# Kernel tuning notes

Hardware: AMD Instinct MI355X
Metric: run time of the kernel (lower is better)

## Reference

```python
import jax, jax.numpy as jnp
import numpy as np

B, F, C = 16384, 256, 256


def setup_inputs() -> dict:
    key = jax.random.key(0)
    ks = jax.random.split(key, 10)
    return {
        "x_t": jax.random.normal(ks[0], (B, F), dtype=jnp.float32),
        "n_t": jax.random.normal(ks[1], (B, C), dtype=jnp.float32),
        "d_t": jax.random.uniform(ks[2], (B, C), dtype=jnp.float32),
        "h_t": jax.random.normal(ks[3], (B, C), dtype=jnp.float32),
        "a_max_t": jax.random.normal(ks[4], (B, C), dtype=jnp.float32),
        "Wu": jax.random.normal(ks[5], (C, F), dtype=jnp.float32) * 0.06,
        "bu": jnp.zeros((C,), dtype=jnp.float32),
        "Wg": jax.random.normal(ks[6], (C, F + C), dtype=jnp.float32) * 0.05,
        "bg": jnp.zeros((C,), dtype=jnp.float32),
        "Wa": jax.random.normal(ks[7], (C, F + C), dtype=jnp.float32) * 0.05,
        "Wd": jax.random.normal(ks[8], (C, F + C), dtype=jnp.float32) * 0.05,
    }


def reference(x_t, n_t, d_t, h_t, a_max_t, Wu, bu, Wg, bg, Wa, Wd):
    # xh_join = cat([x_t, h_t], dim=1) -> [B, F+C]
    xh = jnp.concatenate([x_t, h_t], axis=1)
    u_t = x_t @ Wu.T + bu                      # [B, C]
    g_t = xh @ Wg.T + bg                       # [B, C]
    a_t = xh @ Wa.T                            # [B, C] (no bias)
    z_t = u_t * jnp.tanh(g_t)
    # decay branch (self.decay is an nn.Linear -> always truthy in original)
    decay = jax.nn.sigmoid(xh @ Wd.T)
    e_neg = jnp.exp(-decay)
    a_decay = a_max_t * e_neg
    a_newmax = jnp.maximum(a_decay, a_t)
    exp_diff = jnp.exp(a_max_t - a_newmax)
    exp_scaled = jnp.exp(a_t - a_newmax)
    n_new = n_t * e_neg * exp_diff + z_t * exp_scaled
    d_new = d_t * e_neg * exp_diff + exp_scaled
    h_new = jnp.tanh(n_new / d_new)
    return (n_new, d_new, h_new, a_newmax)
```

## Files before the change

### kernel.cpp

```cpp
#include <hip/hip_runtime.h>
#include <stdint.h>

typedef _Float16 f16x8 __attribute__((ext_vector_type(8)));
typedef __fp16 fp16x2 __attribute__((ext_vector_type(2)));
typedef float f32x4 __attribute__((ext_vector_type(4)));

#define BC (16384 * 256)

__device__ __forceinline__ f16x8 cvt8(f32x4 a, f32x4 b) {
  fp16x2 p0 = __builtin_amdgcn_cvt_pkrtz(a[0], a[1]);
  fp16x2 p1 = __builtin_amdgcn_cvt_pkrtz(a[2], a[3]);
  fp16x2 p2 = __builtin_amdgcn_cvt_pkrtz(b[0], b[1]);
  fp16x2 p3 = __builtin_amdgcn_cvt_pkrtz(b[2], b[3]);
  f16x8 o;
  o[0] = (_Float16)p0[0]; o[1] = (_Float16)p0[1];
  o[2] = (_Float16)p1[0]; o[3] = (_Float16)p1[1];
  o[4] = (_Float16)p2[0]; o[5] = (_Float16)p2[1];
  o[6] = (_Float16)p3[0]; o[7] = (_Float16)p3[1];
  return o;
}

__device__ __forceinline__ float tanh_fast(float v) {
  float a = fminf(fabsf(v), 18.f);
  float t = __expf(2.f * a);
  float r = (t - 1.f) * __builtin_amdgcn_rcpf(t + 1.f);
  return copysignf(r, v);
}

__global__ __launch_bounds__(256) void pack_w(const float* __restrict__ Wu,
                                              const float* __restrict__ Wg,
                                              const float* __restrict__ Wa,
                                              const float* __restrict__ Wd,
                                              _Float16* __restrict__ wsB) {
  int t = blockIdx.x * 256 + threadIdx.x;
  int slot = t & 7;
  int kt = (t >> 3) & 7;
  int row = (t >> 6) & 127;
  int cb = t >> 13;
  int strip = (row >> 4) & 3;
  int wn = row >> 6;
  int t16 = row & 15;
  int c = cb * 32 + wn * 16 + t16;
  int k0 = kt * 64 + (slot ^ (row & 7)) * 8;
  float v[8];
  if (strip == 0) {
    if (k0 < 256) {
      const float* p = Wu + (size_t)c * 256 + k0;
#pragma unroll
      for (int i = 0; i < 8; ++i) v[i] = p[i];
    } else {
#pragma unroll
      for (int i = 0; i < 8; ++i) v[i] = 0.f;
    }
  } else {
    const float* p = (strip == 1 ? Wg : (strip == 2 ? Wa : Wd)) + (size_t)c * 512 + k0;
#pragma unroll
    for (int i = 0; i < 8; ++i) v[i] = p[i];
  }
  f32x4 a = {v[0], v[1], v[2], v[3]};
  f32x4 b = {v[4], v[5], v[6], v[7]};
  *reinterpret_cast<f16x8*>(wsB + (size_t)cb * 65536 + row * 512 + kt * 64 + slot * 8) =
      cvt8(a, b);
}

__global__ __launch_bounds__(256, 3) void rwa_main(
    const float* __restrict__ x, const float* __restrict__ nt_,
    const float* __restrict__ dt_, const float* __restrict__ h,
    const float* __restrict__ amax_, const float* __restrict__ bu,
    const float* __restrict__ bg, const _Float16* __restrict__ wsB,
    float* __restrict__ out) {
  __shared__ __align__(16) _Float16 ldsA[2][64 * 64];
  __shared__ __align__(16) _Float16 ldsB[2][128 * 64];

  const int tid = threadIdx.x;
  const int lane = tid & 63;
  const int l15 = lane & 15;
  const int lg = lane >> 4;
  const int wv = tid >> 6;
  const int wm = wv & 1;
  const int wn = wv >> 1;

  const int bid = blockIdx.x;
  const int xcd = bid & 7;
  const int q = bid >> 3;
  const int cb = q & 7;
  const int rowblk = xcd * 32 + (q >> 3);
  const int row0 = rowblk * 64;

  const int ar = tid >> 2;
  const int aq = tid & 3;

  const _Float16* bsrc0 = wsB + (size_t)cb * 65536 + (tid >> 3) * 512 + (tid & 7) * 8;

  f32x4 acc[2][4] = {};
  f32x4 av[4];

  auto issueA = [&](int kt) {
    const float* sp = (kt < 4 ? x : h) + (size_t)(row0 + ar) * 256 + (kt & 3) * 64 + aq * 16;
#pragma unroll
    for (int i = 0; i < 4; ++i) av[i] = *reinterpret_cast<const f32x4*>(sp + i * 4);
  };
  auto issueB = [&](int buf, int kt) {
#pragma unroll
    for (int i = 0; i < 4; ++i) {
      __builtin_amdgcn_global_load_lds(
          (const __attribute__((address_space(1))) uint32_t*)(bsrc0 + (size_t)kt * 64 + i * 16384),
          (__attribute__((address_space(3))) uint32_t*)(&ldsB[buf][0] + wv * 512 + i * 2048),
          16, 0, 0);
    }
  };
  auto writeA = [&](int buf) {
#pragma unroll
    for (int j = 0; j < 2; ++j) {
      f16x8 o = cvt8(av[2 * j], av[2 * j + 1]);
      const int slot = (aq * 2 + j) ^ (ar & 7);
      *reinterpret_cast<f16x8*>(reinterpret_cast<char*>(&ldsA[buf][0]) + ar * 128 + slot * 16) = o;
    }
  };

  issueA(0);
  issueB(0, 0);
  writeA(0);
  __syncthreads();

#pragma unroll
  for (int kt = 0; kt < 8; ++kt) {
    const int buf = kt & 1;
    if (kt < 7) {
      issueA(kt + 1);
      issueB(buf ^ 1, kt + 1);
    }

    const bool doU = (kt < 4);
    const char* pA = reinterpret_cast<const char*>(&ldsA[buf][0]);
    const char* pB = reinterpret_cast<const char*>(&ldsB[buf][0]);
    const int rswz = (l15 & 7) << 4;
#pragma unroll
    for (int ks = 0; ks < 2; ++ks) {
      f16x8 af[2], bf[4];
#pragma unroll
      for (int mi = 0; mi < 2; ++mi) {
        const int row = wm * 32 + mi * 16 + l15;
        af[mi] = *reinterpret_cast<const f16x8*>(pA + row * 128 + ((ks * 64 + lg * 16) ^ rswz));
      }
#pragma unroll
      for (int s = 0; s < 4; ++s) {
        if (s == 0 && !doU) continue;
        const int pc = wn * 64 + s * 16 + l15;
        bf[s] = *reinterpret_cast<const f16x8*>(pB + pc * 128 + ((ks * 64 + lg * 16) ^ rswz));
      }
#pragma unroll
      for (int s = 0; s < 4; ++s) {
        if (s == 0 && !doU) continue;
#pragma unroll
        for (int mi = 0; mi < 2; ++mi)
          acc[mi][s] = __builtin_amdgcn_mfma_f32_16x16x32_f16(af[mi], bf[s], acc[mi][s], 0, 0, 0);
      }
    }

    if (kt < 7) {
      writeA(buf ^ 1);
      __syncthreads();
    }
  }

  const int c = cb * 32 + wn * 16 + l15;
  const float buv = bu[c];
  const float bgv = bg[c];
#pragma unroll
  for (int mi = 0; mi < 2; ++mi) {
#pragma unroll
    for (int rg = 0; rg < 4; ++rg) {
      const int r = row0 + wm * 32 + mi * 16 + lg * 4 + rg;
      const int idx = r * 256 + c;
      const float u = acc[mi][0][rg] + buv;
      const float gt = acc[mi][1][rg] + bgv;
      const float a = acc[mi][2][rg];
      const float dr = acc[mi][3][rg];
      const float sig = __builtin_amdgcn_rcpf(1.f + __expf(-dr));
      const float z = u * tanh_fast(gt);
      const float am = amax_[idx];
      const float n_old = nt_[idx];
      const float d_old = dt_[idx];
      const float e_neg = __expf(-sig);
      const float a_new = fmaxf(am * e_neg, a);
      const float comm = __expf(am - a_new - sig);
      const float escal = __expf(a - a_new);
      const float n_new = n_old * comm + z * escal;
      const float d_new = d_old * comm + escal;
      const float h_new = tanh_fast(n_new * __builtin_amdgcn_rcpf(d_new));
      out[idx] = n_new;
      out[BC + idx] = d_new;
      out[2 * BC + idx] = h_new;
      out[3 * BC + idx] = a_new;
    }
  }
}

extern "C" void kernel_launch(void* const* d_in, const int* in_sizes, int n_in,
                              void* d_out, int out_size, void* d_ws, size_t ws_size,
                              hipStream_t stream) {
  const float* x_t    = (const float*)d_in[0];
  const float* n_t    = (const float*)d_in[1];
  const float* d_t    = (const float*)d_in[2];
  const float* h_t    = (const float*)d_in[3];
  const float* amax_t = (const float*)d_in[4];
  const float* Wu     = (const float*)d_in[5];
  const float* bu     = (const float*)d_in[6];
  const float* Wg     = (const float*)d_in[7];
  const float* bg     = (const float*)d_in[8];
  const float* Wa     = (const float*)d_in[9];
  const float* Wd     = (const float*)d_in[10];
  float* out = (float*)d_out;

  _Float16* wsB = (_Float16*)d_ws;

  pack_w<<<256, 256, 0, stream>>>(Wu, Wg, Wa, Wd, wsB);
  rwa_main<<<2048, 256, 0, stream>>>(x_t, n_t, d_t, h_t, amax_t, bu, bg, wsB, out);
}
```

Before: 52.88 us.

## Pre-pack activations to swizzled fp16 and stream A tiles via direct-to-LDS loads

Adds a pack_a kernel that converts x and h to fp16 in the swizzled tile layout the GEMM expects, stored in workspace. The main kernel then loads A tiles with global_load_lds like B, replacing the register load, convert and LDS write path. Explicit vmcnt waits and raw barriers replace __syncthreads to overlap the next tile's loads with compute. This costs an extra kernel launch and a full read and write pass over the activations. Each A tile is now read by 8 column-block workgroups in half-size fp16 rather than fp32.

Measured after the change: 51.95 us. No clear change (-1.8%).

```diff
diff --git a/kernel.cpp b/kernel.cpp
--- a/kernel.cpp
+++ b/kernel.cpp
@@ -63,12 +63,27 @@
       cvt8(a, b);
 }
 
+__global__ __launch_bounds__(256) void pack_a(const float* __restrict__ x,
+                                              const float* __restrict__ h,
+                                              _Float16* __restrict__ wsA) {
+  int tid = blockIdx.x * 256 + threadIdx.x;
+  int slot = tid & 7;
+  int row6 = (tid >> 3) & 63;
+  int kt = (tid >> 9) & 7;
+  int rb = tid >> 12;
+  int rowg = rb * 64 + row6;
+  int kin = (kt & 3) * 64 + (slot ^ (row6 & 7)) * 8;
+  const float* src = (kt < 4 ? x : h) + (size_t)rowg * 256 + kin;
+  f32x4 a = *reinterpret_cast<const f32x4*>(src);
+  f32x4 b = *reinterpret_cast<const f32x4*>(src + 4);
+  *reinterpret_cast<f16x8*>(wsA + (size_t)tid * 8) = cvt8(a, b);
+}
+
 __global__ __launch_bounds__(256, 3) void rwa_main(
-    const float* __restrict__ x, const float* __restrict__ nt_,
-    const float* __restrict__ dt_, const float* __restrict__ h,
+    const float* __restrict__ nt_, const float* __restrict__ dt_,
     const float* __restrict__ amax_, const float* __restrict__ bu,
-    const float* __restrict__ bg, const _Float16* __restrict__ wsB,
-    float* __restrict__ out) {
+    const float* __restrict__ bg, const _Float16* __restrict__ wsA,
+    const _Float16* __restrict__ wsB, float* __restrict__ out) {
   __shared__ __align__(16) _Float16 ldsA[2][64 * 64];
   __shared__ __align__(16) _Float16 ldsB[2][128 * 64];
 
@@ -87,20 +102,19 @@
   const int rowblk = xcd * 32 + (q >> 3);
   const int row0 = rowblk * 64;
 
-  const int ar = tid >> 2;
-  const int aq = tid & 3;
-
+  const _Float16* asrc0 = wsA + (size_t)rowblk * 32768 + (size_t)tid * 8;
   const _Float16* bsrc0 = wsB + (size_t)cb * 65536 + (tid >> 3) * 512 + (tid & 7) * 8;
 
   f32x4 acc[2][4] = {};
-  f32x4 av[4];
-
-  auto issueA = [&](int kt) {
-    const float* sp = (kt < 4 ? x : h) + (size_t)(row0 + ar) * 256 + (kt & 3) * 64 + aq * 16;
-#pragma unroll
-    for (int i = 0; i < 4; ++i) av[i] = *reinterpret_cast<const f32x4*>(sp + i * 4);
-  };
-  auto issueB = [&](int buf, int kt) {
+
+  auto stage = [&](int buf, int kt) {
+#pragma unroll
+    for (int i = 0; i < 2; ++i) {
+      __builtin_amdgcn_global_load_lds(
+          (const __attribute__((address_space(1))) uint32_t*)(asrc0 + (size_t)kt * 4096 + i * 2048),
+          (__attribute__((address_space(3))) uint32_t*)(&ldsA[buf][0] + wv * 512 + i * 2048),
+          16, 0, 0);
+    }
 #pragma unroll
     for (int i = 0; i < 4; ++i) {
       __builtin_amdgcn_global_load_lds(
@@ -109,27 +123,21 @@
           16, 0, 0);
     }
   };
-  auto writeA = [&](int buf) {
-#pragma unroll
-    for (int j = 0; j < 2; ++j) {
-      f16x8 o = cvt8(av[2 * j], av[2 * j + 1]);
-      const int slot = (aq * 2 + j) ^ (ar & 7);
-      *reinterpret_cast<f16x8*>(reinterpret_cast<char*>(&ldsA[buf][0]) + ar * 128 + slot * 16) = o;
-    }
-  };
-
-  issueA(0);
-  issueB(0, 0);
-  writeA(0);
-  __syncthreads();
+
+  stage(0, 0);
 
 #pragma unroll
   for (int kt = 0; kt < 8; ++kt) {
     const int buf = kt & 1;
+    if (kt < 7) stage(buf ^ 1, kt + 1);
+
     if (kt < 7) {
-      issueA(kt + 1);
-      issueB(buf ^ 1, kt + 1);
-    }
+      asm volatile("s_waitcnt vmcnt(6)" ::: "memory");
+    } else {
+      asm volatile("s_waitcnt vmcnt(0)" ::: "memory");
+    }
+    __builtin_amdgcn_s_barrier();
+    __builtin_amdgcn_sched_barrier(0);
 
     const bool doU = (kt < 4);
     const char* pA = reinterpret_cast<const char*>(&ldsA[buf][0]);
@@ -159,10 +167,13 @@
     }
 
     if (kt < 7) {
-      writeA(buf ^ 1);
-      __syncthreads();
+      asm volatile("s_waitcnt lgkmcnt(0)" ::: "memory");
+      __builtin_amdgcn_s_barrier();
+      __builtin_amdgcn_sched_barrier(0);
     }
   }
+
+  __builtin_amdgcn_sched_barrier(0);
 
   const int c = cb * 32 + wn * 16 + l15;
   const float buv = bu[c];
@@ -214,7 +225,9 @@
   float* out = (float*)d_out;
 
   _Float16* wsB = (_Float16*)d_ws;
+  _Float16* wsA = (_Float16*)((char*)d_ws + 1048576);
 
   pack_w<<<256, 256, 0, stream>>>(Wu, Wg, Wa, Wd, wsB);
-  rwa_main<<<2048, 256, 0, stream>>>(x_t, n_t, d_t, h_t, amax_t, bu, bg, wsB, out);
-}
+  pack_a<<<4096, 256, 0, stream>>>(x_t, h_t, wsA);
+  rwa_main<<<2048, 256, 0, stream>>>(n_t, d_t, amax_t, bu, bg, wsA, wsB, out);
+}
```
